# Optimization experiments

Measured on AMD Instinct MI355X. Metric: run time of the kernel, lower is better.

## Reference

```python
import jax, jax.numpy as jnp
import numpy as np

N_HEADS = 16
EPS = 1e-4


def setup_inputs() -> dict:
    key = jax.random.key(0)
    ks = jax.random.split(key, 9)
    B, L, E = 4, 4096, 1024
    s = 1.0 / np.sqrt(E)
    return {
        "x": jax.random.normal(ks[0], (B, L, E), dtype=jnp.float32),
        "Wq": jax.random.normal(ks[1], (E, E), dtype=jnp.float32) * s,
        "bq": jax.random.normal(ks[2], (E,), dtype=jnp.float32) * 0.01,
        "Wk": jax.random.normal(ks[3], (E, E), dtype=jnp.float32) * s,
        "bk": jax.random.normal(ks[4], (E,), dtype=jnp.float32) * 0.01,
        "Wv": jax.random.normal(ks[5], (E, E), dtype=jnp.float32) * s,
        "bv": jax.random.normal(ks[6], (E,), dtype=jnp.float32) * 0.01,
        "Wo": jax.random.normal(ks[7], (E, E), dtype=jnp.float32) * s,
        "bo": jax.random.normal(ks[8], (E,), dtype=jnp.float32) * 0.01,
    }


def _cosformer(x, Wq, bq, Wk, bk, Wv, bv, Wo, bo):
    B, L, E = x.shape
    H = N_HEADS
    hd = E // H
    # torch Linear: y = x @ W.T + b; self-attention so q=k=v source is x
    q = jax.nn.relu(jnp.einsum('ble,fe->blf', x, Wq) + bq)
    k = jax.nn.relu(jnp.einsum('ble,fe->blf', x, Wk) + bk)
    v = jnp.einsum('ble,fe->blf', x, Wv) + bv
    # (B, L, E) -> (B*H, L, hd)  [matches torch view(L, B*H, hd).transpose(0,1)]
    def split_heads(t):
        return t.reshape(B, L, H, hd).transpose(0, 2, 1, 3).reshape(B * H, L, hd)
    q, k, v = split_heads(q), split_heads(k), split_heads(v)
    m = L  # src_len == tgt_len
    idx = (np.pi / 2) * jnp.arange(1, m + 1, dtype=jnp.float32) / m  # (m,)
    sin = jnp.sin(idx)[None, :, None]
    cos = jnp.cos(idx)[None, :, None]
    q_ = jnp.concatenate([q * sin, q * cos], axis=-1)  # (BH, L, 2hd)
    k_ = jnp.concatenate([k * sin, k * cos], axis=-1)
    kv = jnp.einsum('nld,nlm->ndm', k_, v)             # (BH, 2hd, hd)
    z = 1.0 / jnp.maximum(jnp.einsum('nld,nd->nl', q_, k_.sum(axis=1)), EPS)
    attn = jnp.einsum('nld,ndm->nlm', q_, kv) * z[:, :, None]  # (BH, L, hd)
    # (B*H, L, hd) -> (B, L, E)
    out = attn.reshape(B, H, L, hd).transpose(0, 2, 1, 3).reshape(B, L, E)
    return jnp.einsum('ble,fe->blf', out, Wo) + bo


def reference(x, Wq, bq, Wk, bk, Wv, bv, Wo, bo):
    return _cosformer(x, Wq, bq, Wk, bk, Wv, bv, Wo, bo)
```

## Files before the change

kernel.cpp:

```cpp
#include <hip/hip_runtime.h>


typedef unsigned short u16;
typedef unsigned int u32;
typedef __attribute__((ext_vector_type(8))) __bf16 bf16x8;
typedef __attribute__((ext_vector_type(4))) float f32x4;

#define PI_HALF 1.57079632679489662f
#define EPS_Z 1e-4f

__device__ __forceinline__ u16 f32_to_bf16(float f) {
    union { float f; unsigned int u; } x; x.f = f;
    unsigned int lsb = (x.u >> 16) & 1u;
    x.u += 0x7fffu + lsb;
    return (u16)(x.u >> 16);
}
__device__ __forceinline__ float bf16_to_f32(u16 u) {
    union { float f; unsigned int u; } x; x.u = ((unsigned int)u) << 16;
    return x.f;
}

typedef __attribute__((address_space(1))) void amdgpu_global_t;
typedef __attribute__((address_space(3))) void amdgpu_lds_t;
__device__ __forceinline__ void async_load16(const u16* g, u16* l) {
    __builtin_amdgcn_global_load_lds((amdgpu_global_t*)g, (amdgpu_lds_t*)l, 16, 0, 0);
}

__global__ __launch_bounds__(256) void cvt_bf16(const float* __restrict__ in,
                                                u16* __restrict__ out, int n4) {
    int i = blockIdx.x * 256 + threadIdx.x;
    if (i >= n4) return;
    float4 f = ((const float4*)in)[i];
    ushort4 o;
    o.x = f32_to_bf16(f.x); o.y = f32_to_bf16(f.y);
    o.z = f32_to_bf16(f.z); o.w = f32_to_bf16(f.w);
    ((ushort4*)out)[i] = o;
}

__global__ __launch_bounds__(256) void cvt_w4(const float* __restrict__ w0,
                                              const float* __restrict__ w1,
                                              const float* __restrict__ w2,
                                              const float* __restrict__ w3,
                                              u16* __restrict__ wcat) {
    const float* src = (blockIdx.y == 0) ? w0 : (blockIdx.y == 1) ? w1
                     : (blockIdx.y == 2) ? w2 : w3;
    u16* dst = wcat + (size_t)blockIdx.y * 1048576;
    int i = blockIdx.x * 256 + threadIdx.x;
    float4 f = ((const float4*)src)[i];
    ushort4 o;
    o.x = f32_to_bf16(f.x); o.y = f32_to_bf16(f.y);
    o.z = f32_to_bf16(f.z); o.w = f32_to_bf16(f.w);
    ((ushort4*)dst)[i] = o;
}

__device__ __forceinline__ void gemm256_core(const u16* __restrict__ Abase,
                                             const u16* __restrict__ Bbase,
                                             u16* As, u16* Bs,
                                             f32x4 (&acc)[8][4]) {
    const int tid  = threadIdx.x;
    const int wave = tid >> 6;
    const int lane = tid & 63;
    const int quad = lane >> 4;
    const int l15  = lane & 15;
    const int wr   = wave >> 2;
    const int wc   = wave & 3;
    const int srow = tid >> 3;
    const int scg  = (tid & 7) ^ (srow & 7);

    const u16* Ag = Abase + ((long)srow << 10) + scg * 8;
    const u16* Bg = Bbase + ((long)srow << 10) + scg * 8;

    auto stage = [&](const u16* g, u16* lb, int hs, int t) {
        async_load16(g + ((long)hs << 16) + (t << 6), lb + hs * 4096);
    };
    auto rdA = [&](const u16* buf, int mf, int kk) -> bf16x8 {
        const int R = wr * 128 + mf * 16 + l15;
        return *(const bf16x8*)(buf + R * 64 + ((kk * 32 + quad * 8) ^ ((R & 7) * 8)));
    };
    auto rdB = [&](const u16* buf, int nf, int kk) -> bf16x8 {
        const int R = wc * 64 + nf * 16 + l15;
        return *(const bf16x8*)(buf + R * 64 + ((kk * 32 + quad * 8) ^ ((R & 7) * 8)));
    };

    bf16x8 a[4][2], b[4][2];
    auto mfma8 = [&](int i0, int j0) {
        __builtin_amdgcn_s_setprio(1);
#pragma unroll
        for (int i = 0; i < 4; ++i)
#pragma unroll
            for (int j = 0; j < 2; ++j)
#pragma unroll
                for (int kk = 0; kk < 2; ++kk)
                    acc[i0 + i][j0 + j] = __builtin_amdgcn_mfma_f32_16x16x32_bf16(
                        a[i][kk], b[j0 + j][kk], acc[i0 + i][j0 + j], 0, 0, 0);
        __builtin_amdgcn_s_setprio(0);
    };

#pragma unroll
    for (int hs = 0; hs < 4; ++hs) stage(Ag, As + wave * 512, hs, 0);
#pragma unroll
    for (int hs = 0; hs < 4; ++hs) stage(Bg, Bs + wave * 512, hs, 0);
#pragma unroll
    for (int hs = 0; hs < 4; ++hs) stage(Ag, As + 16384 + wave * 512, hs, 1);
#pragma unroll
    for (int hs = 0; hs < 4; ++hs) stage(Bg, Bs + 16384 + wave * 512, hs, 1);
    asm volatile("s_waitcnt vmcnt(8)" ::: "memory");
    __builtin_amdgcn_s_barrier();

#pragma unroll 1
    for (int t = 0; t < 16; ++t) {
        const int cur = t & 1;
        const u16* Ab = As + cur * 16384;
        const u16* Bb = Bs + cur * 16384;
        u16* lA = As + cur * 16384 + wave * 512;
        u16* lB = Bs + cur * 16384 + wave * 512;
        const bool pf = (t < 14);

#pragma unroll
        for (int i = 0; i < 4; ++i) { a[i][0] = rdA(Ab, i, 0); a[i][1] = rdA(Ab, i, 1); }
#pragma unroll
        for (int j = 0; j < 2; ++j) { b[j][0] = rdB(Bb, j, 0); b[j][1] = rdB(Bb, j, 1); }
        mfma8(0, 0);
#pragma unroll
        for (int j = 2; j < 4; ++j) { b[j][0] = rdB(Bb, j, 0); b[j][1] = rdB(Bb, j, 1); }
        mfma8(0, 2);
#pragma unroll
        for (int i = 0; i < 4; ++i) { a[i][0] = rdA(Ab, i + 4, 0); a[i][1] = rdA(Ab, i + 4, 1); }
        mfma8(4, 0);

        __builtin_amdgcn_s_barrier();
        asm volatile("" ::: "memory");
        if (pf) {
#pragma unroll
            for (int hs = 0; hs < 4; ++hs) stage(Bg, lB, hs, t + 2);
#pragma unroll
            for (int hs = 0; hs < 4; ++hs) stage(Ag, lA, hs, t + 2);
        }
        mfma8(4, 2);
        if (pf) {
            asm volatile("s_waitcnt vmcnt(8)" ::: "memory");
        } else {
            asm volatile("s_waitcnt vmcnt(0)" ::: "memory");
        }
        __builtin_amdgcn_s_barrier();
        asm volatile("" ::: "memory");
    }
}

__global__ __launch_bounds__(512, 2) void gemm_qkv(const u16* __restrict__ A,
                                                   const u16* __restrict__ Wcat,
                                                   const float* __restrict__ bq,
                                                   const float* __restrict__ bk,
                                                   const float* __restrict__ bv,
                                                   u16* __restrict__ qo,
                                                   u16* __restrict__ ko,
                                                   u16* __restrict__ vo) {
    __shared__ __align__(16) u16 As[32768];
    __shared__ __align__(16) u16 Bs[32768];
    const int bid = blockIdx.x;
    const int swz = (bid & 7) * 96 + (bid >> 3);
    const int bx  = swz / 12;
    const int byy = swz - bx * 12;
    const long tileM = (long)bx * 256;

    f32x4 acc[8][4] = {};
    gemm256_core(A + (tileM << 10), Wcat + ((long)byy << 18), As, Bs, acc);

    const int tid  = (int)threadIdx.x;
    const int wave = tid >> 6;
    const int lane = tid & 63;
    const int quad = lane >> 4, l15 = lane & 15;
    const int wr = wave >> 2, wc = wave & 3;
    const int mat = byy >> 2;
    const float* bias = (mat == 0) ? bq : (mat == 1) ? bk : bv;
    u16* outp = (mat == 0) ? qo : (mat == 1) ? ko : vo;
    const bool relu = (mat < 2);
    const int ncol0 = (byy & 3) * 256;

    const int rloc = tid >> 5;
    const int c8   = (tid & 31) * 8;
#pragma unroll 1
    for (int pass = 0; pass < 2; ++pass) {
        __syncthreads();
        if (wr == pass) {
#pragma unroll
            for (int i = 0; i < 8; ++i)
#pragma unroll
                for (int j = 0; j < 4; ++j) {
                    const int col = wc * 64 + j * 16 + l15;
                    const float bb = bias[ncol0 + col];
#pragma unroll
                    for (int r = 0; r < 4; ++r) {
                        const int row = i * 16 + quad * 4 + r;
                        float v = acc[i][j][r] + bb;
                        if (relu) v = fmaxf(v, 0.0f);
                        As[row * 256 + col] = f32_to_bf16(v);
                    }
                }
        }
        __syncthreads();
        const long gr0 = tileM + pass * 128;
#pragma unroll
        for (int it = 0; it < 8; ++it) {
            const int row = it * 16 + rloc;
            uint4 t4 = *(const uint4*)&As[row * 256 + c8];
            *(uint4*)&outp[(gr0 + row) * 1024 + ncol0 + c8] = t4;
        }
    }
}

__global__ __launch_bounds__(512, 2) void gemm_o(const u16* __restrict__ A,
                                                 const u16* __restrict__ Bw,
                                                 const float* __restrict__ bias,
                                                 float* __restrict__ Cout) {
    __shared__ __align__(16) u16 As[32768];
    __shared__ __align__(16) u16 Bs[32768];
    const int bid = blockIdx.x;
    const int swz = (bid & 7) * 32 + (bid >> 3);
    const long tileM = (long)(swz >> 2) * 256;
    const long tileN = (long)(swz & 3) * 256;

    f32x4 acc[8][4] = {};
    gemm256_core(A + (tileM << 10), Bw + (tileN << 10), As, Bs, acc);

    const int wave = (int)threadIdx.x >> 6;
    const int lane = (int)threadIdx.x & 63;
    const int quad = lane >> 4, l15 = lane & 15;
    const int wr = wave >> 2, wc = wave & 3;
#pragma unroll
    for (int j = 0; j < 4; ++j) {
        const long n = tileN + wc * 64 + j * 16 + l15;
        const float bb = bias[n];
#pragma unroll
        for (int i = 0; i < 8; ++i) {
            const long m0 = tileM + wr * 128 + i * 16 + quad * 4;
#pragma unroll
            for (int r = 0; r < 4; ++r)
                Cout[(m0 + r) * 1024 + n] = acc[i][j][r] + bb;
        }
    }
}

__global__ __launch_bounds__(256) void kv_mfma(const u16* __restrict__ kmat,
                                               const u16* __restrict__ vmat,
                                               float* __restrict__ part) {
    __shared__ u16 Ak[64 * 40];
    __shared__ u16 Bv[64 * 40];
    const int tid = threadIdx.x;
    const int wave = tid >> 6, lane = tid & 63;
    const int quad = lane >> 4, l15 = lane & 15;
    const int head = blockIdx.y;
    const int b = head >> 4, h = head & 15;
    const int l0 = blockIdx.x * 512;
    const int sl = tid >> 3;
    const int sc8 = tid & 7;
    const int scol = sl ^ ((sc8 & 3) << 3);
    const int krow_base = (wave & 1) * 32;
    const bool use_cos = (wave >> 1) != 0;
    const int mbase = wave * 32;

    float sv[8], cv[8];
#pragma unroll
    for (int e = 0; e < 8; e++) {
        float ang = (PI_HALF / 4096.0f) * (float)(l0 + quad * 8 + e + 1);
        sv[e] = sinf(ang); cv[e] = cosf(ang);
    }
    const float cD = 0.9999247018391445f;
    const float sD = 0.0122715382857199f;

    bf16x8 onesf;
#pragma unroll
    for (int e = 0; e < 8; e++)
        onesf[e] = (l15 == 0) ? (__bf16)1.0f : (__bf16)0.0f;

    f32x4 acc[2][5] = {};

    long row = ((long)b * 4096 + l0 + sl) * 1024 + h * 64 + sc8 * 8;
    uint4 kk = *(const uint4*)(kmat + row);
    uint4 vv = *(const uint4*)(vmat + row);

    for (int kt = 0; kt < 16; kt++) {
        uint4 kk_n = {}, vv_n = {};
        if (kt < 15) {
            row += 32 * 1024;
            kk_n = *(const uint4*)(kmat + row);
            vv_n = *(const uint4*)(vmat + row);
        }
        const u16* kp = (const u16*)&kk;
        const u16* vp = (const u16*)&vv;
#pragma unroll
        for (int e = 0; e < 8; e++) {
            const int d = sc8 * 8 + e;
            Ak[d * 40 + scol] = kp[e];
            Bv[d * 40 + scol] = vp[e];
        }
        __syncthreads();

        bf16x8 af[2];
#pragma unroll
        for (int i = 0; i < 2; i++) {
            const int d = krow_base + i * 16 + l15;
            const int q2 = (quad ^ ((d >> 3) & 3)) * 8;
            bf16x8 raw = *(const bf16x8*)&Ak[d * 40 + q2];
            bf16x8 sc;
#pragma unroll
            for (int e = 0; e < 8; e++)
                sc[e] = (__bf16)((float)raw[e] * (use_cos ? cv[e] : sv[e]));
            af[i] = sc;
        }
        bf16x8 bfr[5];
#pragma unroll
        for (int j = 0; j < 4; j++) {
            const int n = j * 16 + l15;
            const int q2 = (quad ^ ((n >> 3) & 3)) * 8;
            bfr[j] = *(const bf16x8*)&Bv[n * 40 + q2];
        }
        bfr[4] = onesf;
#pragma unroll
        for (int i = 0; i < 2; i++)
#pragma unroll
            for (int j = 0; j < 5; j++)
                acc[i][j] = __builtin_amdgcn_mfma_f32_16x16x32_bf16(
                    af[i], bfr[j], acc[i][j], 0, 0, 0);

#pragma unroll
        for (int e = 0; e < 8; e++) {
            const float ns = sv[e] * cD + cv[e] * sD;
            cv[e] = cv[e] * cD - sv[e] * sD;
            sv[e] = ns;
        }
        __syncthreads();
        kk = kk_n; vv = vv_n;
    }

    float* op = part + ((long)blockIdx.x * 64 + head) * 10240;
#pragma unroll
    for (int i = 0; i < 2; i++)
#pragma unroll
        for (int j = 0; j < 5; j++)
#pragma unroll
            for (int r = 0; r < 4; r++)
                op[(mbase + i * 16 + quad * 4 + r) * 80 + j * 16 + l15] = acc[i][j][r];
}

__global__ __launch_bounds__(256) void kv_reduce_t(const float* __restrict__ part,
                                                   u16* __restrict__ Bt) {
    __shared__ float accs[32 * 81];
    const int head = blockIdx.y, d2t = blockIdx.x;
    const float* bp = part + (long)head * 10240 + d2t * 32 * 80;
    for (int idx = threadIdx.x; idx < 2560; idx += 256) {
        float s = 0.0f;
#pragma unroll
        for (int c = 0; c < 8; c++) s += bp[(long)c * 655360 + idx];
        const int d2 = idx / 80, n = idx - d2 * 80;
        accs[d2 * 81 + n] = s;
    }
    __syncthreads();
    for (int idx = threadIdx.x; idx < 2560; idx += 256) {
        const int n = idx >> 5, d2 = idx & 31;
        Bt[(long)head * 10240 + n * 128 + d2t * 32 + d2] = f32_to_bf16(accs[d2 * 81 + n]);
    }
}

__global__ __launch_bounds__(256) void attn_mfma(const u16* __restrict__ qb,
                                                 const u16* __restrict__ Bt,
                                                 u16* __restrict__ merged) {
    __shared__ __align__(16) u16 As[128 * 72];
    __shared__ __align__(16) u16 Bs[80 * 136];
    const int tid = threadIdx.x;
    const int wave = tid >> 6, lane = tid & 63;
    const int quad = lane >> 4, l15 = lane & 15;
    const int head = blockIdx.y;
    const int b = head >> 4, h = head & 15;
    const int tm = blockIdx.x * 128;
    const long b4 = (long)b * 4096;

    for (int c = tid; c < 1024; c += 256) {
        const int row = c >> 3, c8 = c & 7;
        uint4 t = *(const uint4*)(qb + (b4 + tm + row) * 1024 + h * 64 + c8 * 8);
        *(uint4*)&As[row * 72 + c8 * 8] = t;
    }
    for (int c = tid; c < 1280; c += 256) {
        const int row = c >> 4, c16 = c & 15;
        uint4 t = *(const uint4*)(Bt + (long)head * 10240 + row * 128 + c16 * 8);
        *(uint4*)&Bs[row * 136 + c16 * 8] = t;
    }
    const int wm = wave * 32;
    float snl[2], csl[2];
#pragma unroll
    for (int i = 0; i < 2; i++) {
        const int l = tm + wm + i * 16 + l15;
        const float idx = PI_HALF * (float)(l + 1) * (1.0f / 4096.0f);
        snl[i] = sinf(idx); csl[i] = cosf(idx);
    }
    __syncthreads();

    f32x4 acc[2][5] = {};
#pragma unroll
    for (int kb = 0; kb < 4; kb++) {
        const int qc = (kb & 1) * 32 + quad * 8;
        bf16x8 af[2];
#pragma unroll
        for (int i = 0; i < 2; i++) {
            bf16x8 raw = *(const bf16x8*)&As[(wm + i * 16 + l15) * 72 + qc];
            const float s = (kb < 2) ? snl[i] : csl[i];
            bf16x8 sc;
#pragma unroll
            for (int e = 0; e < 8; e++) sc[e] = (__bf16)((float)raw[e] * s);
            af[i] = sc;
        }
        bf16x8 bf[5];
#pragma unroll
        for (int j = 0; j < 5; j++)
            bf[j] = *(const bf16x8*)&Bs[(j * 16 + l15) * 136 + kb * 32 + quad * 8];
#pragma unroll
        for (int i = 0; i < 2; i++)
#pragma unroll
            for (int j = 0; j < 5; j++)
                acc[i][j] = __builtin_amdgcn_mfma_f32_16x16x32_bf16(
                    af[i], bf[j], acc[i][j], 0, 0, 0);
    }

    __syncthreads();
#pragma unroll
    for (int i = 0; i < 2; i++) {
        float z[4];
#pragma unroll
        for (int r = 0; r < 4; r++) {
            const float den = __shfl(acc[i][4][r], lane & 0x30, 64);
            z[r] = 1.0f / fmaxf(den, EPS_Z);
        }
#pragma unroll
        for (int j = 0; j < 4; j++)
#pragma unroll
            for (int r = 0; r < 4; r++) {
                const int row = wm + i * 16 + quad * 4 + r;
                As[row * 64 + j * 16 + l15] = f32_to_bf16(acc[i][j][r] * z[r]);
            }
    }
    __syncthreads();
    const int rloc = tid >> 3, c8 = (tid & 7) * 8;
#pragma unroll
    for (int it = 0; it < 4; ++it) {
        const int row = it * 32 + rloc;
        uint4 t4 = *(const uint4*)&As[row * 64 + c8];
        *(uint4*)&merged[(b4 + tm + row) * 1024 + h * 64 + c8] = t4;
    }
}

extern "C" void kernel_launch(void* const* d_in, const int* in_sizes, int n_in,
                              void* d_out, int out_size, void* d_ws, size_t ws_size,
                              hipStream_t stream) {
    (void)in_sizes; (void)n_in; (void)out_size; (void)ws_size;
    const float* x  = (const float*)d_in[0];
    const float* Wq = (const float*)d_in[1];
    const float* bq = (const float*)d_in[2];
    const float* Wk = (const float*)d_in[3];
    const float* bk = (const float*)d_in[4];
    const float* Wv = (const float*)d_in[5];
    const float* bv = (const float*)d_in[6];
    const float* Wo = (const float*)d_in[7];
    const float* bo = (const float*)d_in[8];
    float* out = (float*)d_out;

    const int M = 16384, E = 1024;
    char* ws = (char*)d_ws;
    const size_t MB = 1048576;
    u16* xb   = (u16*)(ws);
    u16* qb   = (u16*)(ws + 32 * MB);
    u16* kb   = (u16*)(ws + 64 * MB);
    u16* vb   = (u16*)(ws + 96 * MB);
    u16* wcat = (u16*)(ws + 128 * MB);
    u16* wob  = wcat + 3 * (size_t)E * E;
    u16* Btb  = (u16*)(ws + 136 * MB);
    float* part = (float*)xb;
    u16* mergedb = kb;

    cvt_bf16<<<dim3(M * E / 4 / 256), dim3(256), 0, stream>>>(x, xb, M * E / 4);
    cvt_w4<<<dim3(E * E / 4 / 256, 4), dim3(256), 0, stream>>>(Wq, Wk, Wv, Wo, wcat);

    gemm_qkv<<<dim3(768), dim3(512), 0, stream>>>(xb, wcat, bq, bk, bv, qb, kb, vb);

    kv_mfma<<<dim3(8, 64), dim3(256), 0, stream>>>(kb, vb, part);
    kv_reduce_t<<<dim3(4, 64), dim3(256), 0, stream>>>(part, Btb);
    attn_mfma<<<dim3(32, 64), dim3(256), 0, stream>>>(qb, Btb, mergedb);

    gemm_o<<<dim3(256), dim3(512), 0, stream>>>(mergedb, wob, bo, out);
}
```

Measured before the change: 343.9 us.

## Merge conversion kernels, double kv_mfma k-step, halve attn_mfma grid with two tiles per block

The two fp32-to-bf16 conversion kernels are folded into one launch that covers both x and the four weight matrices. kv_mfma now stages 64 sequence rows per iteration instead of 32, running two MFMAs per accumulator and keeping a second sin/cos rotation set, which halves the number of barriers and loop trips. attn_mfma processes two 128-row tiles per block so the per-head kv matrix is loaded into shared memory once and reused, at the cost of half as many blocks in the grid. The extra registers and the larger shared tile may reduce occupancy.

```diff
diff --git a/kernel.cpp b/kernel.cpp
--- a/kernel.cpp
+++ b/kernel.cpp
@@ -15,10 +15,6 @@
     x.u += 0x7fffu + lsb;
     return (u16)(x.u >> 16);
 }
-__device__ __forceinline__ float bf16_to_f32(u16 u) {
-    union { float f; unsigned int u; } x; x.u = ((unsigned int)u) << 16;
-    return x.f;
-}
 
 typedef __attribute__((address_space(1))) void amdgpu_global_t;
 typedef __attribute__((address_space(3))) void amdgpu_lds_t;
@@ -26,26 +22,27 @@
     __builtin_amdgcn_global_load_lds((amdgpu_global_t*)g, (amdgpu_lds_t*)l, 16, 0, 0);
 }
 
-__global__ __launch_bounds__(256) void cvt_bf16(const float* __restrict__ in,
-                                                u16* __restrict__ out, int n4) {
-    int i = blockIdx.x * 256 + threadIdx.x;
-    if (i >= n4) return;
-    float4 f = ((const float4*)in)[i];
-    ushort4 o;
-    o.x = f32_to_bf16(f.x); o.y = f32_to_bf16(f.y);
-    o.z = f32_to_bf16(f.z); o.w = f32_to_bf16(f.w);
-    ((ushort4*)out)[i] = o;
-}
-
-__global__ __launch_bounds__(256) void cvt_w4(const float* __restrict__ w0,
-                                              const float* __restrict__ w1,
-                                              const float* __restrict__ w2,
-                                              const float* __restrict__ w3,
-                                              u16* __restrict__ wcat) {
-    const float* src = (blockIdx.y == 0) ? w0 : (blockIdx.y == 1) ? w1
-                     : (blockIdx.y == 2) ? w2 : w3;
-    u16* dst = wcat + (size_t)blockIdx.y * 1048576;
-    int i = blockIdx.x * 256 + threadIdx.x;
+__global__ __launch_bounds__(256) void cvt_all(const float* __restrict__ x,
+                                               const float* __restrict__ w0,
+                                               const float* __restrict__ w1,
+                                               const float* __restrict__ w2,
+                                               const float* __restrict__ w3,
+                                               u16* __restrict__ xb,
+                                               u16* __restrict__ wcat) {
+    const int bid = blockIdx.x;
+    const float* src;
+    u16* dst;
+    int i;
+    if (bid < 16384) {
+        src = x; dst = xb;
+        i = bid * 256 + threadIdx.x;
+    } else {
+        const int wb = bid - 16384;
+        const int wsel = wb >> 10;
+        src = (wsel == 0) ? w0 : (wsel == 1) ? w1 : (wsel == 2) ? w2 : w3;
+        dst = wcat + (size_t)wsel * 1048576;
+        i = (wb & 1023) * 256 + threadIdx.x;
+    }
     float4 f = ((const float4*)src)[i];
     ushort4 o;
     o.x = f32_to_bf16(f.x); o.y = f32_to_bf16(f.y);
@@ -244,8 +241,8 @@
 __global__ __launch_bounds__(256) void kv_mfma(const u16* __restrict__ kmat,
                                                const u16* __restrict__ vmat,
                                                float* __restrict__ part) {
-    __shared__ u16 Ak[64 * 40];
-    __shared__ u16 Bv[64 * 40];
+    __shared__ u16 Ak[64 * 72];
+    __shared__ u16 Bv[64 * 72];
     const int tid = threadIdx.x;
     const int wave = tid >> 6, lane = tid & 63;
     const int quad = lane >> 4, l15 = lane & 15;
@@ -259,14 +256,16 @@
     const bool use_cos = (wave >> 1) != 0;
     const int mbase = wave * 32;
 
-    float sv[8], cv[8];
+    float sv[8], cv[8], s2[8], c2[8];
 #pragma unroll
     for (int e = 0; e < 8; e++) {
         float ang = (PI_HALF / 4096.0f) * (float)(l0 + quad * 8 + e + 1);
         sv[e] = sinf(ang); cv[e] = cosf(ang);
-    }
-    const float cD = 0.9999247018391445f;
-    const float sD = 0.0122715382857199f;
+        float ang2 = ang + (PI_HALF / 4096.0f) * 32.0f;
+        s2[e] = sinf(ang2); c2[e] = cosf(ang2);
+    }
+    const float cD = 0.99969881869620422f;
+    const float sD = 0.02454122852291229f;
 
     bf16x8 onesf;
 #pragma unroll
@@ -276,61 +275,85 @@
     f32x4 acc[2][5] = {};
 
     long row = ((long)b * 4096 + l0 + sl) * 1024 + h * 64 + sc8 * 8;
-    uint4 kk = *(const uint4*)(kmat + row);
-    uint4 vv = *(const uint4*)(vmat + row);
-
-    for (int kt = 0; kt < 16; kt++) {
-        uint4 kk_n = {}, vv_n = {};
-        if (kt < 15) {
-            row += 32 * 1024;
-            kk_n = *(const uint4*)(kmat + row);
-            vv_n = *(const uint4*)(vmat + row);
-        }
-        const u16* kp = (const u16*)&kk;
-        const u16* vp = (const u16*)&vv;
-#pragma unroll
-        for (int e = 0; e < 8; e++) {
-            const int d = sc8 * 8 + e;
-            Ak[d * 40 + scol] = kp[e];
-            Bv[d * 40 + scol] = vp[e];
-        }
-        __syncthreads();
-
-        bf16x8 af[2];
+    uint4 kkA = *(const uint4*)(kmat + row);
+    uint4 vvA = *(const uint4*)(vmat + row);
+    uint4 kkB = *(const uint4*)(kmat + row + 32 * 1024);
+    uint4 vvB = *(const uint4*)(vmat + row + 32 * 1024);
+
+#pragma unroll 1
+    for (int kt = 0; kt < 8; kt++) {
+        uint4 kkA_n = {}, vvA_n = {}, kkB_n = {}, vvB_n = {};
+        if (kt < 7) {
+            row += 64 * 1024;
+            kkA_n = *(const uint4*)(kmat + row);
+            vvA_n = *(const uint4*)(vmat + row);
+            kkB_n = *(const uint4*)(kmat + row + 32 * 1024);
+            vvB_n = *(const uint4*)(vmat + row + 32 * 1024);
+        }
+        {
+            const u16* kp = (const u16*)&kkA;
+            const u16* vp = (const u16*)&vvA;
+            const u16* kp2 = (const u16*)&kkB;
+            const u16* vp2 = (const u16*)&vvB;
+#pragma unroll
+            for (int e = 0; e < 8; e++) {
+                const int d = sc8 * 8 + e;
+                Ak[d * 72 + scol]      = kp[e];
+                Bv[d * 72 + scol]      = vp[e];
+                Ak[d * 72 + scol + 32] = kp2[e];
+                Bv[d * 72 + scol + 32] = vp2[e];
+            }
+        }
+        __syncthreads();
+
+        bf16x8 af[2][2];
 #pragma unroll
         for (int i = 0; i < 2; i++) {
             const int d = krow_base + i * 16 + l15;
             const int q2 = (quad ^ ((d >> 3) & 3)) * 8;
-            bf16x8 raw = *(const bf16x8*)&Ak[d * 40 + q2];
-            bf16x8 sc;
-#pragma unroll
-            for (int e = 0; e < 8; e++)
-                sc[e] = (__bf16)((float)raw[e] * (use_cos ? cv[e] : sv[e]));
-            af[i] = sc;
-        }
-        bf16x8 bfr[5];
+#pragma unroll
+            for (int kk = 0; kk < 2; kk++) {
+                bf16x8 raw = *(const bf16x8*)&Ak[d * 72 + kk * 32 + q2];
+                bf16x8 sc;
+#pragma unroll
+                for (int e = 0; e < 8; e++) {
+                    const float s = use_cos ? (kk ? c2[e] : cv[e])
+                                            : (kk ? s2[e] : sv[e]);
+                    sc[e] = (__bf16)((float)raw[e] * s);
+                }
+                af[i][kk] = sc;
+            }
+        }
+        bf16x8 bfr[5][2];
 #pragma unroll
         for (int j = 0; j < 4; j++) {
             const int n = j * 16 + l15;
             const int q2 = (quad ^ ((n >> 3) & 3)) * 8;
-            bfr[j] = *(const bf16x8*)&Bv[n * 40 + q2];
-        }
-        bfr[4] = onesf;
+            bfr[j][0] = *(const bf16x8*)&Bv[n * 72 + q2];
+            bfr[j][1] = *(const bf16x8*)&Bv[n * 72 + 32 + q2];
+        }
+        bfr[4][0] = onesf; bfr[4][1] = onesf;
 #pragma unroll
         for (int i = 0; i < 2; i++)
 #pragma unroll
-            for (int j = 0; j < 5; j++)
+            for (int j = 0; j < 5; j++) {
                 acc[i][j] = __builtin_amdgcn_mfma_f32_16x16x32_bf16(
-                    af[i], bfr[j], acc[i][j], 0, 0, 0);
+                    af[i][0], bfr[j][0], acc[i][j], 0, 0, 0);
+                acc[i][j] = __builtin_amdgcn_mfma_f32_16x16x32_bf16(
+                    af[i][1], bfr[j][1], acc[i][j], 0, 0, 0);
+            }
 
 #pragma unroll
         for (int e = 0; e < 8; e++) {
-            const float ns = sv[e] * cD + cv[e] * sD;
+            float ns = sv[e] * cD + cv[e] * sD;
             cv[e] = cv[e] * cD - sv[e] * sD;
             sv[e] = ns;
-        }
-        __syncthreads();
-        kk = kk_n; vv = vv_n;
+            ns = s2[e] * cD + c2[e] * sD;
+            c2[e] = c2[e] * cD - s2[e] * sD;
+            s2[e] = ns;
+        }
+        __syncthreads();
+        kkA = kkA_n; vvA = vvA_n; kkB = kkB_n; vvB = vvB_n;
     }
 
     float* op = part + ((long)blockIdx.x * 64 + head) * 10240;
@@ -372,79 +395,85 @@
     const int quad = lane >> 4, l15 = lane & 15;
     const int head = blockIdx.y;
     const int b = head >> 4, h = head & 15;
-    const int tm = blockIdx.x * 128;
+    const int tm0 = blockIdx.x * 256;
     const long b4 = (long)b * 4096;
-
-    for (int c = tid; c < 1024; c += 256) {
-        const int row = c >> 3, c8 = c & 7;
-        uint4 t = *(const uint4*)(qb + (b4 + tm + row) * 1024 + h * 64 + c8 * 8);
-        *(uint4*)&As[row * 72 + c8 * 8] = t;
-    }
+    const int wm = wave * 32;
+
     for (int c = tid; c < 1280; c += 256) {
         const int row = c >> 4, c16 = c & 15;
         uint4 t = *(const uint4*)(Bt + (long)head * 10240 + row * 128 + c16 * 8);
         *(uint4*)&Bs[row * 136 + c16 * 8] = t;
     }
-    const int wm = wave * 32;
-    float snl[2], csl[2];
-#pragma unroll
-    for (int i = 0; i < 2; i++) {
-        const int l = tm + wm + i * 16 + l15;
-        const float idx = PI_HALF * (float)(l + 1) * (1.0f / 4096.0f);
-        snl[i] = sinf(idx); csl[i] = cosf(idx);
-    }
-    __syncthreads();
-
-    f32x4 acc[2][5] = {};
-#pragma unroll
-    for (int kb = 0; kb < 4; kb++) {
-        const int qc = (kb & 1) * 32 + quad * 8;
-        bf16x8 af[2];
+
+#pragma unroll 1
+    for (int half = 0; half < 2; ++half) {
+        const int tm = tm0 + half * 128;
+        __syncthreads();
+        for (int c = tid; c < 1024; c += 256) {
+            const int row = c >> 3, c8 = c & 7;
+            uint4 t = *(const uint4*)(qb + (b4 + tm + row) * 1024 + h * 64 + c8 * 8);
+            *(uint4*)&As[row * 72 + c8 * 8] = t;
+        }
+        float snl[2], csl[2];
 #pragma unroll
         for (int i = 0; i < 2; i++) {
-            bf16x8 raw = *(const bf16x8*)&As[(wm + i * 16 + l15) * 72 + qc];
-            const float s = (kb < 2) ? snl[i] : csl[i];
-            bf16x8 sc;
-#pragma unroll
-            for (int e = 0; e < 8; e++) sc[e] = (__bf16)((float)raw[e] * s);
-            af[i] = sc;
-        }
-        bf16x8 bf[5];
-#pragma unroll
-        for (int j = 0; j < 5; j++)
-            bf[j] = *(const bf16x8*)&Bs[(j * 16 + l15) * 136 + kb * 32 + quad * 8];
-#pragma unroll
-        for (int i = 0; i < 2; i++)
+            const int l = tm + wm + i * 16 + l15;
+            const float idx = PI_HALF * (float)(l + 1) * (1.0f / 4096.0f);
+            snl[i] = sinf(idx); csl[i] = cosf(idx);
+        }
+        __syncthreads();
+
+        f32x4 acc[2][5] = {};
+#pragma unroll
+        for (int kb = 0; kb < 4; kb++) {
+            const int qc = (kb & 1) * 32 + quad * 8;
+            bf16x8 af[2];
+#pragma unroll
+            for (int i = 0; i < 2; i++) {
+                bf16x8 raw = *(const bf16x8*)&As[(wm + i * 16 + l15) * 72 + qc];
+                const float s = (kb < 2) ? snl[i] : csl[i];
+                bf16x8 sc;
+#pragma unroll
+                for (int e = 0; e < 8; e++) sc[e] = (__bf16)((float)raw[e] * s);
+                af[i] = sc;
+            }
+            bf16x8 bf[5];
 #pragma unroll
             for (int j = 0; j < 5; j++)
-                acc[i][j] = __builtin_amdgcn_mfma_f32_16x16x32_bf16(
-                    af[i], bf[j], acc[i][j], 0, 0, 0);
-    }
-
-    __syncthreads();
-#pragma unroll
-    for (int i = 0; i < 2; i++) {
-        float z[4];
-#pragma unroll
-        for (int r = 0; r < 4; r++) {
-            const float den = __shfl(acc[i][4][r], lane & 0x30, 64);
-            z[r] = 1.0f / fmaxf(den, EPS_Z);
-        }
-#pragma unroll
-        for (int j = 0; j < 4; j++)
+                bf[j] = *(const bf16x8*)&Bs[(j * 16 + l15) * 136 + kb * 32 + quad * 8];
+#pragma unroll
+            for (int i = 0; i < 2; i++)
+#pragma unroll
+                for (int j = 0; j < 5; j++)
+                    acc[i][j] = __builtin_amdgcn_mfma_f32_16x16x32_bf16(
+                        af[i], bf[j], acc[i][j], 0, 0, 0);
+        }
+
+        __syncthreads();
+#pragma unroll
+        for (int i = 0; i < 2; i++) {
+            float z[4];
 #pragma unroll
             for (int r = 0; r < 4; r++) {
-                const int row = wm + i * 16 + quad * 4 + r;
-                As[row * 64 + j * 16 + l15] = f32_to_bf16(acc[i][j][r] * z[r]);
+                const float den = __shfl(acc[i][4][r], lane & 0x30, 64);
+                z[r] = 1.0f / fmaxf(den, EPS_Z);
             }
-    }
-    __syncthreads();
-    const int rloc = tid >> 3, c8 = (tid & 7) * 8;
-#pragma unroll
-    for (int it = 0; it < 4; ++it) {
-        const int row = it * 32 + rloc;
-        uint4 t4 = *(const uint4*)&As[row * 64 + c8];
-        *(uint4*)&merged[(b4 + tm + row) * 1024 + h * 64 + c8] = t4;
+#pragma unroll
+            for (int j = 0; j < 4; j++)
+#pragma unroll
+                for (int r = 0; r < 4; r++) {
+                    const int row = wm + i * 16 + quad * 4 + r;
+                    As[row * 64 + j * 16 + l15] = f32_to_bf16(acc[i][j][r] * z[r]);
+                }
+        }
+        __syncthreads();
+        const int rloc = tid >> 3, c8o = (tid & 7) * 8;
+#pragma unroll
+        for (int it = 0; it < 4; ++it) {
+            const int row = it * 32 + rloc;
+            uint4 t4 = *(const uint4*)&As[row * 64 + c8o];
+            *(uint4*)&merged[(b4 + tm + row) * 1024 + h * 64 + c8o] = t4;
+        }
     }
 }
 
@@ -463,7 +492,7 @@
     const float* bo = (const float*)d_in[8];
     float* out = (float*)d_out;
 
-    const int M = 16384, E = 1024;
+    const int E = 1024;
     char* ws = (char*)d_ws;
     const size_t MB = 1048576;
     u16* xb   = (u16*)(ws);
@@ -476,14 +505,13 @@
     float* part = (float*)xb;
     u16* mergedb = kb;
 
-    cvt_bf16<<<dim3(M * E / 4 / 256), dim3(256), 0, stream>>>(x, xb, M * E / 4);
-    cvt_w4<<<dim3(E * E / 4 / 256, 4), dim3(256), 0, stream>>>(Wq, Wk, Wv, Wo, wcat);
+    cvt_all<<<dim3(20480), dim3(256), 0, stream>>>(x, Wq, Wk, Wv, Wo, xb, wcat);
 
     gemm_qkv<<<dim3(768), dim3(512), 0, stream>>>(xb, wcat, bq, bk, bv, qb, kb, vb);
 
     kv_mfma<<<dim3(8, 64), dim3(256), 0, stream>>>(kb, vb, part);
     kv_reduce_t<<<dim3(4, 64), dim3(256), 0, stream>>>(part, Btb);
-    attn_mfma<<<dim3(32, 64), dim3(256), 0, stream>>>(qb, Btb, mergedb);
+    attn_mfma<<<dim3(16, 64), dim3(256), 0, stream>>>(qb, Btb, mergedb);
 
     gemm_o<<<dim3(256), dim3(512), 0, stream>>>(mergedb, wob, bo, out);
 }
```

Result: no change. 341.1 us (-0.8%).
